# Kernel optimization log

Measured on AMD Instinct MI355X. Metric: run time of the kernel, lower is better.

## Reference

```python
import jax, jax.numpy as jnp
import numpy as np

D = 256  # rst_input_dim


def _gru_cell(x, h, W_ih, W_hh, b_ih, b_hh):
    # x, h: (..., D); W_*: (3D, D); PyTorch GRU gate order: r, z, n
    gi = x @ W_ih.T + b_ih          # (..., 3D)
    gh = h @ W_hh.T + b_hh
    i_r, i_z, i_n = jnp.split(gi, 3, axis=-1)
    h_r, h_z, h_n = jnp.split(gh, 3, axis=-1)
    r = jax.nn.sigmoid(i_r + h_r)
    z = jax.nn.sigmoid(i_z + h_z)
    n = jnp.tanh(i_n + r * h_n)
    return (1.0 - z) * n + z * h


def setup_inputs() -> dict:
    key = jax.random.key(0)
    ks = jax.random.split(key, 5)
    B, L = 32, 4096
    s = 1.0 / np.sqrt(D)
    return {
        "leaf_embeds": jax.random.normal(ks[0], (B, L, D), dtype=jnp.float32),
        "W_ih": jax.random.normal(ks[1], (3 * D, D), dtype=jnp.float32) * s,
        "W_hh": jax.random.normal(ks[2], (3 * D, D), dtype=jnp.float32) * s,
        "b_ih": jax.random.normal(ks[3], (3 * D,), dtype=jnp.float32) * s,
        "b_hh": jax.random.normal(ks[4], (3 * D,), dtype=jnp.float32) * s,
    }


def reference(leaf_embeds, W_ih, W_hh, b_ih, b_hh):
    # Post-order traversal of a perfect binary tree, batched level-by-level
    # (classic tree-RNN same-depth batching). Leaves: embed = EDU embedding,
    # hidden = zeros. Internal node: h0 = mean(h_left, h_right); run GRU over
    # the 2-step sequence [left_embed, right_embed]; out = mean of the two
    # GRU outputs; returned hidden = final GRU hidden.
    embeds = leaf_embeds                      # (B, N, D)
    hs = jnp.zeros_like(leaf_embeds)          # (B, N, D)
    n = embeds.shape[1]
    while n > 1:
        xL, xR = embeds[:, 0::2], embeds[:, 1::2]   # (B, n/2, D)
        hL, hR = hs[:, 0::2], hs[:, 1::2]
        h0 = 0.5 * (hL + hR)                         # mean of child hiddens
        h1 = _gru_cell(xL, h0, W_ih, W_hh, b_ih, b_hh)
        h2 = _gru_cell(xR, h1, W_ih, W_hh, b_ih, b_hh)
        embeds = 0.5 * (h1 + h2)                     # mean over seq outputs
        hs = h2
        n //= 2
    return embeds[:, 0]                              # (B, D): root embedding
```

## Files before the change

kernel.cpp:

```cpp
#include <hip/hip_runtime.h>
#include <hip/hip_bf16.h>
#include <stdint.h>

typedef _Float16 f16x8 __attribute__((ext_vector_type(8)));
typedef _Float16 f16x4 __attribute__((ext_vector_type(4)));
typedef float    f32x4 __attribute__((ext_vector_type(4)));

#define GLDS16(gptr, lptr) \
  __builtin_amdgcn_global_load_lds((const __attribute__((address_space(1))) void*)(gptr), \
                                   (__attribute__((address_space(3))) void*)(lptr), 16, 0, 0)

#define WAITV(N) asm volatile("s_waitcnt vmcnt(" #N ")" ::: "memory")

__device__ __forceinline__ int tile_off(int rb, int c, int sub) {
    return ((rb * 4 + c) * 8 + sub) * 512;
}

__global__ __launch_bounds__(256) void prepack_weights(
    const float* __restrict__ Wih, const float* __restrict__ Whh,
    const float* __restrict__ bih, const float* __restrict__ bhh,
    _Float16* __restrict__ WP, float* __restrict__ BC)
{
    if (blockIdx.x == 2048) {
        int i = threadIdx.x;
        BC[i]       = bih[i] + bhh[i];
        BC[256 + i] = bih[256 + i] + bhh[256 + i];
        BC[512 + i] = bih[512 + i];
        BC[768 + i] = bhh[512 + i];
        return;
    }
    int idx = blockIdx.x * 256 + threadIdx.x;
    int j   = idx & 7;
    int nl  = (idx >> 3) & 63;
    int sub = (idx >> 9) & 7;
    int g   = (idx >> 12) & 3;
    int d0b = (idx >> 14) & 3;
    int c   = idx >> 16;
    int k = c * 64 + sub * 8 + j;
    int d = d0b * 64 + nl;
    float v = 0.f;
    if (g == 0)      v = (k < 256) ? Wih[d * 256 + k]         : Whh[d * 256 + (k - 256)];
    else if (g == 1) v = (k < 256) ? Wih[(256 + d) * 256 + k] : Whh[(256 + d) * 256 + (k - 256)];
    else if (g == 2) v = (k < 256) ? Wih[(512 + d) * 256 + k] : 0.f;
    else             v = (k >= 256) ? Whh[(512 + d) * 256 + (k - 256)] : 0.f;
    WP[idx] = (_Float16)v;
}

__global__ __launch_bounds__(256) void convert_split(
    const float* __restrict__ leaf, _Float16* __restrict__ XE, _Float16* __restrict__ XO)
{
    int g = blockIdx.x * 256 + threadIdx.x;
    int u = g & 31;
    int row = g >> 5;
    const float* src = leaf + (size_t)row * 256 + u * 8;
    float4 a = *(const float4*)src;
    float4 b = *(const float4*)(src + 4);
    f16x8 p;
    p[0] = (_Float16)a.x; p[1] = (_Float16)a.y; p[2] = (_Float16)a.z; p[3] = (_Float16)a.w;
    p[4] = (_Float16)b.x; p[5] = (_Float16)b.y; p[6] = (_Float16)b.z; p[7] = (_Float16)b.w;
    int ro = row >> 1;
    _Float16* dst = (row & 1) ? XO : XE;
    *(f16x8*)(dst + tile_off(ro >> 6, u >> 3, u & 7) + (ro & 63) * 8) = p;
}

template<int MT, bool SWIZ>
__global__ __launch_bounds__(256, (MT == 8) ? 2 : 3) void gru_cell(
    const _Float16* __restrict__ Xsrc,
    const _Float16* __restrict__ Hsrc,
    const _Float16* __restrict__ WP,
    const float* __restrict__ BC,
    _Float16* __restrict__ Hout,
    _Float16* __restrict__ Ee, _Float16* __restrict__ Eo, _Float16* __restrict__ HP,
    int M)
{
    (void)M;
    constexpr int NBUF = (MT == 8) ? 2 : 3;
    constexpr int AROW = MT * 16 * 8;
    constexpr int ASZ  = 8 * AROW;
    __shared__ __align__(16) _Float16 Alds[NBUF * ASZ];

    const int tid  = threadIdx.x;
    int bm, d0b;
    if (SWIZ) {
        int xcd = blockIdx.x & 7, slot = blockIdx.x >> 3;
        d0b = slot & 3;
        bm  = (slot >> 2) * 8 + xcd;
    } else {
        bm = blockIdx.x >> 2; d0b = blockIdx.x & 3;
    }
    const int wave = tid >> 6, lane = tid & 63;
    const int quad = lane >> 4, lo = lane & 15;

    const bool has_h = (Hsrc != nullptr);
    const int nch = has_h ? 8 : 4;

    f32x4 acc[MT][4];
#pragma unroll
    for (int a = 0; a < MT; ++a)
#pragma unroll
        for (int b = 0; b < 4; ++b) acc[a][b] = (f32x4){0.f, 0.f, 0.f, 0.f};
    f16x4 hinvh[MT];

    auto loadB = [&](int c, f16x8 (&bb)[2][3]) {
        const size_t cb = (size_t)(c * 4 + d0b) * 4;
        const int col = (wave * 16 + lo) * 8;
#pragma unroll
        for (int ks = 0; ks < 2; ++ks) {
            const int subb = ks * 4 + quad;
#pragma unroll
            for (int slot = 0; slot < 3; ++slot) {
                int g = (slot == 2) ? ((c < 4) ? 2 : 3) : slot;
                bb[ks][slot] = *(const f16x8*)(WP + ((cb + g) * 8 + subb) * 512 + col);
            }
        }
    };

    auto issueA = [&](int c, int buf) {
        const _Float16* base = (c < 4) ? Xsrc : Hsrc;
        const int cc = c & 3;
        _Float16* Ab = Alds + buf * ASZ;
        constexpr int ND = MT / 2;
#pragma unroll
        for (int i = 0; i < ND; ++i) {
            int ai = wave * ND + i;
            int sub = (MT == 8) ? (ai >> 1) : ai;
            int mh  = (MT == 8) ? (ai & 1) : 0;
            GLDS16(base + tile_off(bm * (MT / 4) + mh, cc, sub) + lane * 8,
                   Ab + sub * AROW + mh * 512);
        }
    };

    auto compute = [&](int c, int buf, f16x8 (&bb)[2][3]) {
        const _Float16* Ab = Alds + buf * ASZ;
#pragma unroll
        for (int ks = 0; ks < 2; ++ks) {
            const int subb = ks * 4 + quad;
#pragma unroll
            for (int mt = 0; mt < MT; ++mt) {
                f16x8 a = *(const f16x8*)(Ab + subb * AROW + (mt * 16 + lo) * 8);
                acc[mt][0] = __builtin_amdgcn_mfma_f32_16x16x32_f16(a, bb[ks][0], acc[mt][0], 0, 0, 0);
                acc[mt][1] = __builtin_amdgcn_mfma_f32_16x16x32_f16(a, bb[ks][1], acc[mt][1], 0, 0, 0);
                if (c < 4)
                    acc[mt][2] = __builtin_amdgcn_mfma_f32_16x16x32_f16(a, bb[ks][2], acc[mt][2], 0, 0, 0);
                else
                    acc[mt][3] = __builtin_amdgcn_mfma_f32_16x16x32_f16(a, bb[ks][2], acc[mt][3], 0, 0, 0);
            }
        }
        if (has_h && c == 4 + d0b) {
            const int colw = wave * 16 + lo;
            const int sub = colw >> 3, j = colw & 7;
#pragma unroll
            for (int mt = 0; mt < MT; ++mt)
#pragma unroll
                for (int r = 0; r < 4; ++r)
                    hinvh[mt][r] = Ab[sub * AROW + (mt * 16 + quad * 4 + r) * 8 + j];
        }
    };

    if constexpr (MT == 8) {
        issueA(0, 0);
        for (int c = 0; c < nch; ++c) {
            __syncthreads();
            f16x8 bb[2][3];
            loadB(c, bb);
            __builtin_amdgcn_sched_barrier(0);
            if (c + 1 < nch) issueA(c + 1, (c + 1) & 1);
            compute(c, c & 1, bb);
        }
    } else {
        issueA(0, 0); issueA(1, 1);
        for (int c = 0; c < nch; ++c) {
            if (c < nch - 1) WAITV(2); else WAITV(0);
            __builtin_amdgcn_s_barrier();
            __builtin_amdgcn_sched_barrier(0);
            f16x8 bb[2][3];
            loadB(c, bb);
            __builtin_amdgcn_sched_barrier(0);
            if (c + 2 < nch) issueA(c + 2, (c + 2) % 3);
            compute(c, c % 3, bb);
        }
    }

    const int ld = wave * 16 + lo;
    const int d  = d0b * 64 + ld;
    const float brz0 = BC[d];
    const float brz1 = BC[256 + d];
    const float bni  = BC[512 + d];
    const float bnh  = BC[768 + d];
    constexpr int SROW = 72;
    constexpr int PR   = MT * 8;
    __syncthreads();
#pragma unroll
    for (int mt = 0; mt < MT; ++mt) {
        const int lr0 = mt * 16 + quad * 4;
        float hq[4];
#pragma unroll
        for (int r = 0; r < 4; ++r) {
            float hin = has_h ? (float)hinvh[mt][r] : 0.f;
            float rg = 1.f / (1.f + __expf(-(acc[mt][0][r] + brz0)));
            float zg = 1.f / (1.f + __expf(-(acc[mt][1][r] + brz1)));
            float ex = __expf(2.f * (acc[mt][2][r] + bni + rg * (acc[mt][3][r] + bnh)));
            float nv = 1.f - 2.f / (ex + 1.f);
            hq[r] = (1.f - zg) * nv + zg * hin;
            int lr = lr0 + r;
            if (Hout) {
                Alds[lr * SROW + ld] = (_Float16)hq[r];
            } else {
                Alds[(((lr & 1) * PR) + (lr >> 1)) * SROW + ld] =
                    (_Float16)(0.5f * (hin + hq[r]));
            }
        }
        if (!Hout) {
            Alds[(2 * PR + (lr0 >> 1)) * SROW + ld]     = (_Float16)(0.5f * (hq[0] + hq[1]));
            Alds[(2 * PR + (lr0 >> 1) + 1) * SROW + ld] = (_Float16)(0.5f * (hq[2] + hq[3]));
        }
    }
    __syncthreads();

    if (Hout) {
        constexpr int NU = MT * 128;
#pragma unroll
        for (int i = 0; i < NU / 256; ++i) {
            int uid = i * 256 + tid;
            int r = uid & 63, sub = (uid >> 6) & 7, mh = uid >> 9;
            f16x8 v = *(const f16x8*)&Alds[(mh * 64 + r) * SROW + sub * 8];
            *(f16x8*)(Hout + tile_off(bm * (MT / 4) + mh, d0b, sub) + r * 8) = v;
        }
    } else {
        constexpr int NU = 3 * PR * 8;
        const int rbE  = (MT == 8) ? bm : (bm >> 1);
        const int roff = (MT == 8) ? 0 : (bm & 1) * 32;
#pragma unroll
        for (int i = 0; i < NU / 256; ++i) {
            int uid = i * 256 + tid;
            int pr   = uid & (PR - 1);
            int rest = uid / PR;
            int sub = rest & 7, buf = rest >> 3;
            f16x8 v = *(const f16x8*)&Alds[(buf * PR + pr) * SROW + sub * 8];
            _Float16* dst = (buf == 0) ? Ee : (buf == 1) ? Eo : HP;
            *(f16x8*)(dst + tile_off(rbE, d0b, sub) + (roff + pr) * 8) = v;
        }
    }
}

__global__ __launch_bounds__(256) void final_out(
    const _Float16* __restrict__ XE, const _Float16* __restrict__ XO,
    float* __restrict__ out)
{
    int i = blockIdx.x * 256 + threadIdx.x;
    int j = i >> 8, col = i & 255;
    const _Float16* src = (j & 1) ? XO : XE;
    int r = j >> 1;
    out[i] = (float)src[tile_off(0, col >> 6, (col >> 3) & 7) + r * 8 + (col & 7)];
}

extern "C" void kernel_launch(void* const* d_in, const int* in_sizes, int n_in,
                              void* d_out, int out_size, void* d_ws, size_t ws_size,
                              hipStream_t stream) {
    const float* leaf = (const float*)d_in[0];
    const float* Wih  = (const float*)d_in[1];
    const float* Whh  = (const float*)d_in[2];
    const float* bih  = (const float*)d_in[3];
    const float* bhh  = (const float*)d_in[4];

    char* ws = (char*)d_ws;
    _Float16* WPp = (_Float16*)ws;
    _Float16* XAe = (_Float16*)(ws + (1ull  << 20));
    _Float16* XAo = (_Float16*)(ws + (33ull << 20));
    _Float16* XBe = (_Float16*)(ws + (65ull << 20));
    _Float16* XBo = (_Float16*)(ws + (81ull << 20));
    _Float16* H1  = (_Float16*)(ws + (97ull << 20));
    _Float16* HPb = (_Float16*)(ws + (129ull << 20));
    float*    BCp = (float*)(ws + (145ull << 20));

    prepack_weights<<<2049, 256, 0, stream>>>(Wih, Whh, bih, bhh, WPp, BCp);
    convert_split<<<16384, 256, 0, stream>>>(leaf, XAe, XAo);

    _Float16 *XeC = XAe, *XoC = XAo, *XeN = XBe, *XoN = XBo;
    const _Float16* hp = nullptr;
    int M = 65536;
    for (int lev = 0; lev < 12; ++lev) {
        if (M >= 8192) {
            int grid = (M / 128) * 4;
            gru_cell<8, true><<<grid, 256, 0, stream>>>(XeC, hp, WPp, BCp,
                                                        H1, nullptr, nullptr, nullptr, M);
            gru_cell<8, true><<<grid, 256, 0, stream>>>(XoC, H1, WPp, BCp,
                                                        nullptr, XeN, XoN, HPb, M);
        } else {
            int nbm = (M + 63) / 64;
            int grid = nbm * 4;
            if ((nbm & 7) == 0) {
                gru_cell<4, true><<<grid, 256, 0, stream>>>(XeC, hp, WPp, BCp,
                                                            H1, nullptr, nullptr, nullptr, M);
                gru_cell<4, true><<<grid, 256, 0, stream>>>(XoC, H1, WPp, BCp,
                                                            nullptr, XeN, XoN, HPb, M);
            } else {
                gru_cell<4, false><<<grid, 256, 0, stream>>>(XeC, hp, WPp, BCp,
                                                             H1, nullptr, nullptr, nullptr, M);
                gru_cell<4, false><<<grid, 256, 0, stream>>>(XoC, H1, WPp, BCp,
                                                             nullptr, XeN, XoN, HPb, M);
            }
        }
        hp = HPb;
        _Float16* t;
        t = XeC; XeC = XeN; XeN = t;
        t = XoC; XoC = XoN; XoN = t;
        M >>= 1;
    }
    final_out<<<32, 256, 0, stream>>>(XeC, XoC, (float*)d_out);
}
```

Baseline: 662.9 us.

## Fuse both GRU steps into one kernel for small tree levels

For levels 4 through 11, the two gru_cell launches per level are replaced by a single gru_tail16 kernel. Each block handles 16 rows across all 256 output columns, keeps h1 in LDS and registers, and runs the second GRU step without writing h1 to global memory. The last level writes the fp32 root output directly, so final_out is removed. This halves the launches and global round-trips on the latency-bound tail levels, at the cost of small grids (down to one block) that each read the full weight matrix per block.

```diff
diff --git a/kernel.cpp b/kernel.cpp
--- a/kernel.cpp
+++ b/kernel.cpp
@@ -64,7 +64,7 @@
 }
 
 template<int MT, bool SWIZ>
-__global__ __launch_bounds__(256, (MT == 8) ? 2 : 3) void gru_cell(
+__global__ __launch_bounds__(256, 2) void gru_cell(
     const _Float16* __restrict__ Xsrc,
     const _Float16* __restrict__ Hsrc,
     const _Float16* __restrict__ WP,
@@ -74,10 +74,9 @@
     int M)
 {
     (void)M;
-    constexpr int NBUF = (MT == 8) ? 2 : 3;
     constexpr int AROW = MT * 16 * 8;
     constexpr int ASZ  = 8 * AROW;
-    __shared__ __align__(16) _Float16 Alds[NBUF * ASZ];
+    __shared__ __align__(16) _Float16 Alds[2 * ASZ];
 
     const int tid  = threadIdx.x;
     int bm, d0b;
@@ -123,8 +122,7 @@
 #pragma unroll
         for (int i = 0; i < ND; ++i) {
             int ai = wave * ND + i;
-            int sub = (MT == 8) ? (ai >> 1) : ai;
-            int mh  = (MT == 8) ? (ai & 1) : 0;
+            int sub = ai >> 1, mh = ai & 1;
             GLDS16(base + tile_off(bm * (MT / 4) + mh, cc, sub) + lane * 8,
                    Ab + sub * AROW + mh * 512);
         }
@@ -157,28 +155,14 @@
         }
     };
 
-    if constexpr (MT == 8) {
-        issueA(0, 0);
-        for (int c = 0; c < nch; ++c) {
-            __syncthreads();
-            f16x8 bb[2][3];
-            loadB(c, bb);
-            __builtin_amdgcn_sched_barrier(0);
-            if (c + 1 < nch) issueA(c + 1, (c + 1) & 1);
-            compute(c, c & 1, bb);
-        }
-    } else {
-        issueA(0, 0); issueA(1, 1);
-        for (int c = 0; c < nch; ++c) {
-            if (c < nch - 1) WAITV(2); else WAITV(0);
-            __builtin_amdgcn_s_barrier();
-            __builtin_amdgcn_sched_barrier(0);
-            f16x8 bb[2][3];
-            loadB(c, bb);
-            __builtin_amdgcn_sched_barrier(0);
-            if (c + 2 < nch) issueA(c + 2, (c + 2) % 3);
-            compute(c, c % 3, bb);
-        }
+    issueA(0, 0);
+    for (int c = 0; c < nch; ++c) {
+        __syncthreads();
+        f16x8 bb[2][3];
+        loadB(c, bb);
+        __builtin_amdgcn_sched_barrier(0);
+        if (c + 1 < nch) issueA(c + 1, (c + 1) & 1);
+        compute(c, c & 1, bb);
     }
 
     const int ld = wave * 16 + lo;
@@ -228,8 +212,6 @@
         }
     } else {
         constexpr int NU = 3 * PR * 8;
-        const int rbE  = (MT == 8) ? bm : (bm >> 1);
-        const int roff = (MT == 8) ? 0 : (bm & 1) * 32;
 #pragma unroll
         for (int i = 0; i < NU / 256; ++i) {
             int uid = i * 256 + tid;
@@ -238,20 +220,178 @@
             int sub = rest & 7, buf = rest >> 3;
             f16x8 v = *(const f16x8*)&Alds[(buf * PR + pr) * SROW + sub * 8];
             _Float16* dst = (buf == 0) ? Ee : (buf == 1) ? Eo : HP;
-            *(f16x8*)(dst + tile_off(rbE, d0b, sub) + (roff + pr) * 8) = v;
-        }
-    }
-}
-
-__global__ __launch_bounds__(256) void final_out(
-    const _Float16* __restrict__ XE, const _Float16* __restrict__ XO,
-    float* __restrict__ out)
+            *(f16x8*)(dst + tile_off(bm, d0b, sub) + pr * 8) = v;
+        }
+    }
+}
+
+__global__ __launch_bounds__(256, 1) void gru_tail16(
+    const _Float16* __restrict__ Xe, const _Float16* __restrict__ Xo,
+    const _Float16* __restrict__ HPs,
+    const _Float16* __restrict__ WP, const float* __restrict__ BC,
+    _Float16* __restrict__ Ee, _Float16* __restrict__ Eo,
+    _Float16* __restrict__ HPd, float* __restrict__ out)
 {
-    int i = blockIdx.x * 256 + threadIdx.x;
-    int j = i >> 8, col = i & 255;
-    const _Float16* src = (j & 1) ? XO : XE;
-    int r = j >> 1;
-    out[i] = (float)src[tile_off(0, col >> 6, (col >> 3) & 7) + r * 8 + (col & 7)];
+    __shared__ __align__(16) _Float16 A[3][1024];
+    __shared__ __align__(16) _Float16 H1i[4][1024];
+
+    const int tid  = threadIdx.x;
+    const int wave = tid >> 6, lane = tid & 63;
+    const int quad = lane >> 4, lo = lane & 15;
+    const int bid  = blockIdx.x;
+    const int m0 = bid * 16, rb = m0 >> 6, ro = m0 & 63;
+
+    float brz0[4], brz1[4], bni[4], bnh[4];
+#pragma unroll
+    for (int nt = 0; nt < 4; ++nt) {
+        int d = wave * 64 + nt * 16 + lo;
+        brz0[nt] = BC[d];       brz1[nt] = BC[256 + d];
+        bni[nt]  = BC[512 + d]; bnh[nt]  = BC[768 + d];
+    }
+
+    f32x4 acc[4][4];
+    auto zacc = [&] {
+#pragma unroll
+        for (int nt = 0; nt < 4; ++nt)
+#pragma unroll
+            for (int g = 0; g < 4; ++g) acc[nt][g] = (f32x4){0.f, 0.f, 0.f, 0.f};
+    };
+
+    auto issueA = [&](const _Float16* base, int cc, int buf) {
+        const int i = wave >> 1;
+        GLDS16(base + tile_off(rb, cc, i * 4 + (lane >> 4)) + (ro + (lane & 15)) * 8,
+               &A[buf][i * 512]);
+    };
+
+    auto loadB = [&](int c, f16x8 (&bb)[2][4][3]) {
+#pragma unroll
+        for (int ks = 0; ks < 2; ++ks) {
+            const int subq = ks * 4 + quad;
+            const _Float16* wb = WP + (size_t)((c * 4 + wave) * 4) * 4096 + subq * 512;
+#pragma unroll
+            for (int nt = 0; nt < 4; ++nt) {
+                const int colb = (nt * 16 + lo) * 8;
+                bb[ks][nt][0] = *(const f16x8*)(wb + colb);
+                bb[ks][nt][1] = *(const f16x8*)(wb + 4096 + colb);
+                bb[ks][nt][2] = *(const f16x8*)(wb + ((c < 4) ? 2 : 3) * 4096 + colb);
+            }
+        }
+    };
+
+    auto mfmaC = [&](int c, const _Float16* Ab, f16x8 (&bb)[2][4][3]) {
+#pragma unroll
+        for (int ks = 0; ks < 2; ++ks) {
+            const int subq = ks * 4 + quad;
+            f16x8 a = *(const f16x8*)(Ab + subq * 128 + lo * 8);
+#pragma unroll
+            for (int nt = 0; nt < 4; ++nt) {
+                acc[nt][0] = __builtin_amdgcn_mfma_f32_16x16x32_f16(a, bb[ks][nt][0], acc[nt][0], 0, 0, 0);
+                acc[nt][1] = __builtin_amdgcn_mfma_f32_16x16x32_f16(a, bb[ks][nt][1], acc[nt][1], 0, 0, 0);
+                if (c < 4)
+                    acc[nt][2] = __builtin_amdgcn_mfma_f32_16x16x32_f16(a, bb[ks][nt][2], acc[nt][2], 0, 0, 0);
+                else
+                    acc[nt][3] = __builtin_amdgcn_mfma_f32_16x16x32_f16(a, bb[ks][nt][2], acc[nt][3], 0, 0, 0);
+            }
+        }
+    };
+
+    zacc();
+    float hin[4][4];
+    issueA(Xe, 0, 0);
+    issueA(Xe, 1, 1);
+    for (int c = 0; c < 8; ++c) {
+        if (c < 7) WAITV(1); else WAITV(0);
+        __builtin_amdgcn_s_barrier();
+        __builtin_amdgcn_sched_barrier(0);
+        f16x8 bb[2][4][3];
+        loadB(c, bb);
+        __builtin_amdgcn_sched_barrier(0);
+        if (c + 2 < 8) {
+            int cn = c + 2;
+            issueA((cn < 4) ? Xe : HPs, cn & 3, cn % 3);
+        }
+        const _Float16* Ab = A[c % 3];
+        mfmaC(c, Ab, bb);
+        if (c == 4 + wave) {
+#pragma unroll
+            for (int nt = 0; nt < 4; ++nt) {
+                const int sb = nt * 2 + (lo >> 3), j = lo & 7;
+#pragma unroll
+                for (int r = 0; r < 4; ++r)
+                    hin[nt][r] = (float)Ab[sb * 128 + (quad * 4 + r) * 8 + j];
+            }
+        }
+    }
+
+    __syncthreads();
+    float h1v[4][4];
+#pragma unroll
+    for (int nt = 0; nt < 4; ++nt) {
+        const int sb = nt * 2 + (lo >> 3), j = lo & 7;
+#pragma unroll
+        for (int r = 0; r < 4; ++r) {
+            float rg = 1.f / (1.f + __expf(-(acc[nt][0][r] + brz0[nt])));
+            float zg = 1.f / (1.f + __expf(-(acc[nt][1][r] + brz1[nt])));
+            float ex = __expf(2.f * (acc[nt][2][r] + bni[nt] + rg * (acc[nt][3][r] + bnh[nt])));
+            float nv = 1.f - 2.f / (ex + 1.f);
+            float h  = (1.f - zg) * nv + zg * hin[nt][r];
+            h1v[nt][r] = h;
+            H1i[wave][sb * 128 + (quad * 4 + r) * 8 + j] = (_Float16)h;
+        }
+    }
+    __syncthreads();
+
+    zacc();
+    issueA(Xo, 0, 0);
+    issueA(Xo, 1, 1);
+    for (int c = 0; c < 4; ++c) {
+        if (c < 3) WAITV(1); else WAITV(0);
+        __builtin_amdgcn_s_barrier();
+        __builtin_amdgcn_sched_barrier(0);
+        f16x8 bb[2][4][3];
+        loadB(c, bb);
+        __builtin_amdgcn_sched_barrier(0);
+        if (c + 2 < 4) issueA(Xo, c + 2, (c + 2) % 3);
+        mfmaC(c, A[c % 3], bb);
+    }
+#pragma unroll
+    for (int c = 4; c < 8; ++c) {
+        f16x8 bb[2][4][3];
+        loadB(c, bb);
+        mfmaC(c, &H1i[c - 4][0], bb);
+    }
+
+#pragma unroll
+    for (int nt = 0; nt < 4; ++nt) {
+        const int sb = nt * 2 + (lo >> 3), j = lo & 7;
+        float h2[4];
+#pragma unroll
+        for (int r = 0; r < 4; ++r) {
+            float rg = 1.f / (1.f + __expf(-(acc[nt][0][r] + brz0[nt])));
+            float zg = 1.f / (1.f + __expf(-(acc[nt][1][r] + brz1[nt])));
+            float ex = __expf(2.f * (acc[nt][2][r] + bni[nt] + rg * (acc[nt][3][r] + bnh[nt])));
+            float nv = 1.f - 2.f / (ex + 1.f);
+            h2[r] = (1.f - zg) * nv + zg * h1v[nt][r];
+        }
+        if (out) {
+#pragma unroll
+            for (int r = 0; r < 4; ++r)
+                out[(size_t)(m0 + quad * 4 + r) * 256 + wave * 64 + nt * 16 + lo] =
+                    0.5f * (h1v[nt][r] + h2[r]);
+        } else {
+            const int rbE   = bid >> 3;
+            const int rbase = (bid & 7) * 8 + quad * 2;
+            const int toff  = tile_off(rbE, wave, sb);
+#pragma unroll
+            for (int r = 0; r < 4; ++r) {
+                _Float16* dst = (r & 1) ? Eo : Ee;
+                dst[toff + (rbase + (r >> 1)) * 8 + j] =
+                    (_Float16)(0.5f * (h1v[nt][r] + h2[r]));
+            }
+            HPd[toff + rbase * 8 + j]       = (_Float16)(0.5f * (h2[0] + h2[1]));
+            HPd[toff + (rbase + 1) * 8 + j] = (_Float16)(0.5f * (h2[2] + h2[3]));
+        }
+    }
 }
 
 extern "C" void kernel_launch(void* const* d_in, const int* in_sizes, int n_in,
@@ -270,6 +410,7 @@
     _Float16* XBe = (_Float16*)(ws + (65ull << 20));
     _Float16* XBo = (_Float16*)(ws + (81ull << 20));
     _Float16* H1  = (_Float16*)(ws + (97ull << 20));
+    _Float16* HP2 = (_Float16*)(ws + (113ull << 20));
     _Float16* HPb = (_Float16*)(ws + (129ull << 20));
     float*    BCp = (float*)(ws + (145ull << 20));
 
@@ -279,33 +420,29 @@
     _Float16 *XeC = XAe, *XoC = XAo, *XeN = XBe, *XoN = XBo;
     const _Float16* hp = nullptr;
     int M = 65536;
-    for (int lev = 0; lev < 12; ++lev) {
-        if (M >= 8192) {
-            int grid = (M / 128) * 4;
-            gru_cell<8, true><<<grid, 256, 0, stream>>>(XeC, hp, WPp, BCp,
-                                                        H1, nullptr, nullptr, nullptr, M);
-            gru_cell<8, true><<<grid, 256, 0, stream>>>(XoC, H1, WPp, BCp,
-                                                        nullptr, XeN, XoN, HPb, M);
-        } else {
-            int nbm = (M + 63) / 64;
-            int grid = nbm * 4;
-            if ((nbm & 7) == 0) {
-                gru_cell<4, true><<<grid, 256, 0, stream>>>(XeC, hp, WPp, BCp,
-                                                            H1, nullptr, nullptr, nullptr, M);
-                gru_cell<4, true><<<grid, 256, 0, stream>>>(XoC, H1, WPp, BCp,
-                                                            nullptr, XeN, XoN, HPb, M);
-            } else {
-                gru_cell<4, false><<<grid, 256, 0, stream>>>(XeC, hp, WPp, BCp,
-                                                             H1, nullptr, nullptr, nullptr, M);
-                gru_cell<4, false><<<grid, 256, 0, stream>>>(XoC, H1, WPp, BCp,
-                                                             nullptr, XeN, XoN, HPb, M);
-            }
-        }
+    for (int lev = 0; lev < 4; ++lev) {
+        int grid = (M / 128) * 4;
+        gru_cell<8, true><<<grid, 256, 0, stream>>>(XeC, hp, WPp, BCp,
+                                                    H1, nullptr, nullptr, nullptr, M);
+        gru_cell<8, true><<<grid, 256, 0, stream>>>(XoC, H1, WPp, BCp,
+                                                    nullptr, XeN, XoN, HPb, M);
         hp = HPb;
         _Float16* t;
         t = XeC; XeC = XeN; XeN = t;
         t = XoC; XoC = XoN; XoN = t;
         M >>= 1;
     }
-    final_out<<<32, 256, 0, stream>>>(XeC, XoC, (float*)d_out);
-}
+
+    for (int lev = 4; lev <= 11; ++lev) {
+        int nb = (65536 >> lev) / 16;
+        _Float16* Xe = (lev & 1) ? XBe : XAe;
+        _Float16* Xo = (lev & 1) ? XBo : XAo;
+        _Float16* De = (lev & 1) ? XAe : XBe;
+        _Float16* Do = (lev & 1) ? XAo : XBo;
+        _Float16* HPsrc = (lev & 1) ? HP2 : HPb;
+        _Float16* HPdst = (lev & 1) ? HPb : HP2;
+        float* op = (lev == 11) ? (float*)d_out : nullptr;
+        gru_tail16<<<nb, 256, 0, stream>>>(Xe, Xo, HPsrc, WPp, BCp,
+                                           De, Do, HPdst, op);
+    }
+}
```

Result: slower. 751.1 us (+13.3%).

## Fuse small tree levels into one persistent kernel with grid barriers

Applied to the files above, without the earlier changes.

Levels 4 through 11, where the row count is small, now run inside a single persistent kernel of 256 blocks. Blocks synchronize between GRU half-steps with an atomic-counter grid barrier, and the final output copy is folded into the same kernel. This removes roughly 17 small kernel launches and their launch gaps, which dominate when work per level is tiny. The cost is spin-wait barrier overhead and a reliance on all 256 blocks being co-resident. HP buffers now ping-pong to avoid read/write hazards within the fused kernel.

```diff
diff --git a/kernel.cpp b/kernel.cpp
--- a/kernel.cpp
+++ b/kernel.cpp
@@ -19,7 +19,7 @@
 __global__ __launch_bounds__(256) void prepack_weights(
     const float* __restrict__ Wih, const float* __restrict__ Whh,
     const float* __restrict__ bih, const float* __restrict__ bhh,
-    _Float16* __restrict__ WP, float* __restrict__ BC)
+    _Float16* __restrict__ WP, float* __restrict__ BC, int* __restrict__ CNT)
 {
     if (blockIdx.x == 2048) {
         int i = threadIdx.x;
@@ -27,6 +27,7 @@
         BC[256 + i] = bih[256 + i] + bhh[256 + i];
         BC[512 + i] = bih[512 + i];
         BC[768 + i] = bhh[512 + i];
+        if (i == 0) *CNT = 0;
         return;
     }
     int idx = blockIdx.x * 256 + threadIdx.x;
@@ -64,7 +65,7 @@
 }
 
 template<int MT, bool SWIZ>
-__global__ __launch_bounds__(256, (MT == 8) ? 2 : 3) void gru_cell(
+__global__ __launch_bounds__(256, 2) void gru_cell(
     const _Float16* __restrict__ Xsrc,
     const _Float16* __restrict__ Hsrc,
     const _Float16* __restrict__ WP,
@@ -74,10 +75,9 @@
     int M)
 {
     (void)M;
-    constexpr int NBUF = (MT == 8) ? 2 : 3;
     constexpr int AROW = MT * 16 * 8;
     constexpr int ASZ  = 8 * AROW;
-    __shared__ __align__(16) _Float16 Alds[NBUF * ASZ];
+    __shared__ __align__(16) _Float16 Alds[2 * ASZ];
 
     const int tid  = threadIdx.x;
     int bm, d0b;
@@ -123,8 +123,7 @@
 #pragma unroll
         for (int i = 0; i < ND; ++i) {
             int ai = wave * ND + i;
-            int sub = (MT == 8) ? (ai >> 1) : ai;
-            int mh  = (MT == 8) ? (ai & 1) : 0;
+            int sub = ai >> 1, mh = ai & 1;
             GLDS16(base + tile_off(bm * (MT / 4) + mh, cc, sub) + lane * 8,
                    Ab + sub * AROW + mh * 512);
         }
@@ -157,28 +156,14 @@
         }
     };
 
-    if constexpr (MT == 8) {
-        issueA(0, 0);
-        for (int c = 0; c < nch; ++c) {
-            __syncthreads();
-            f16x8 bb[2][3];
-            loadB(c, bb);
-            __builtin_amdgcn_sched_barrier(0);
-            if (c + 1 < nch) issueA(c + 1, (c + 1) & 1);
-            compute(c, c & 1, bb);
-        }
-    } else {
-        issueA(0, 0); issueA(1, 1);
-        for (int c = 0; c < nch; ++c) {
-            if (c < nch - 1) WAITV(2); else WAITV(0);
-            __builtin_amdgcn_s_barrier();
-            __builtin_amdgcn_sched_barrier(0);
-            f16x8 bb[2][3];
-            loadB(c, bb);
-            __builtin_amdgcn_sched_barrier(0);
-            if (c + 2 < nch) issueA(c + 2, (c + 2) % 3);
-            compute(c, c % 3, bb);
-        }
+    issueA(0, 0);
+    for (int c = 0; c < nch; ++c) {
+        __syncthreads();
+        f16x8 bb[2][3];
+        loadB(c, bb);
+        __builtin_amdgcn_sched_barrier(0);
+        if (c + 1 < nch) issueA(c + 1, (c + 1) & 1);
+        compute(c, c & 1, bb);
     }
 
     const int ld = wave * 16 + lo;
@@ -228,8 +213,152 @@
         }
     } else {
         constexpr int NU = 3 * PR * 8;
-        const int rbE  = (MT == 8) ? bm : (bm >> 1);
-        const int roff = (MT == 8) ? 0 : (bm & 1) * 32;
+#pragma unroll
+        for (int i = 0; i < NU / 256; ++i) {
+            int uid = i * 256 + tid;
+            int pr   = uid & (PR - 1);
+            int rest = uid / PR;
+            int sub = rest & 7, buf = rest >> 3;
+            f16x8 v = *(const f16x8*)&Alds[(buf * PR + pr) * SROW + sub * 8];
+            _Float16* dst = (buf == 0) ? Ee : (buf == 1) ? Eo : HP;
+            *(f16x8*)(dst + tile_off(bm, d0b, sub) + pr * 8) = v;
+        }
+    }
+}
+
+__device__ void cell4(const _Float16* __restrict__ Xsrc,
+                      const _Float16* __restrict__ Hsrc,
+                      const _Float16* __restrict__ WP,
+                      const float* __restrict__ BC,
+                      _Float16* Hout, _Float16* Ee, _Float16* Eo, _Float16* HP,
+                      int bm, int d0b, int tid, _Float16* Alds)
+{
+    constexpr int MT   = 4;
+    constexpr int AROW = 512;
+    constexpr int ASZ  = 4096;
+    const int wave = tid >> 6, lane = tid & 63;
+    const int quad = lane >> 4, lo = lane & 15;
+
+    f32x4 acc[MT][4];
+#pragma unroll
+    for (int a = 0; a < MT; ++a)
+#pragma unroll
+        for (int b = 0; b < 4; ++b) acc[a][b] = (f32x4){0.f, 0.f, 0.f, 0.f};
+    f16x4 hinvh[MT];
+
+    auto loadB = [&](int c, f16x8 (&bb)[2][3]) {
+        const size_t cb = (size_t)(c * 4 + d0b) * 4;
+        const int col = (wave * 16 + lo) * 8;
+#pragma unroll
+        for (int ks = 0; ks < 2; ++ks) {
+            const int subb = ks * 4 + quad;
+#pragma unroll
+            for (int slot = 0; slot < 3; ++slot) {
+                int g = (slot == 2) ? ((c < 4) ? 2 : 3) : slot;
+                bb[ks][slot] = *(const f16x8*)(WP + ((cb + g) * 8 + subb) * 512 + col);
+            }
+        }
+    };
+
+    auto issueA = [&](int c, int buf) {
+        const _Float16* base = (c < 4) ? Xsrc : Hsrc;
+        const int cc = c & 3;
+        _Float16* Ab = Alds + buf * ASZ;
+#pragma unroll
+        for (int i = 0; i < 2; ++i) {
+            int sub = wave * 2 + i;
+            GLDS16(base + tile_off(bm, cc, sub) + lane * 8, Ab + sub * AROW);
+        }
+    };
+
+    auto compute = [&](int c, int buf, f16x8 (&bb)[2][3]) {
+        const _Float16* Ab = Alds + buf * ASZ;
+#pragma unroll
+        for (int ks = 0; ks < 2; ++ks) {
+            const int subb = ks * 4 + quad;
+#pragma unroll
+            for (int mt = 0; mt < MT; ++mt) {
+                f16x8 a = *(const f16x8*)(Ab + subb * AROW + (mt * 16 + lo) * 8);
+                acc[mt][0] = __builtin_amdgcn_mfma_f32_16x16x32_f16(a, bb[ks][0], acc[mt][0], 0, 0, 0);
+                acc[mt][1] = __builtin_amdgcn_mfma_f32_16x16x32_f16(a, bb[ks][1], acc[mt][1], 0, 0, 0);
+                if (c < 4)
+                    acc[mt][2] = __builtin_amdgcn_mfma_f32_16x16x32_f16(a, bb[ks][2], acc[mt][2], 0, 0, 0);
+                else
+                    acc[mt][3] = __builtin_amdgcn_mfma_f32_16x16x32_f16(a, bb[ks][2], acc[mt][3], 0, 0, 0);
+            }
+        }
+        if (c == 4 + d0b) {
+            const int colw = wave * 16 + lo;
+            const int sub = colw >> 3, j = colw & 7;
+#pragma unroll
+            for (int mt = 0; mt < MT; ++mt)
+#pragma unroll
+                for (int r = 0; r < 4; ++r)
+                    hinvh[mt][r] = Ab[sub * AROW + (mt * 16 + quad * 4 + r) * 8 + j];
+        }
+    };
+
+    issueA(0, 0); issueA(1, 1);
+    for (int c = 0; c < 8; ++c) {
+        if (c < 7) WAITV(2); else WAITV(0);
+        __builtin_amdgcn_s_barrier();
+        __builtin_amdgcn_sched_barrier(0);
+        f16x8 bb[2][3];
+        loadB(c, bb);
+        __builtin_amdgcn_sched_barrier(0);
+        if (c + 2 < 8) issueA(c + 2, (c + 2) % 3);
+        compute(c, c % 3, bb);
+    }
+
+    const int ld = wave * 16 + lo;
+    const int d  = d0b * 64 + ld;
+    const float brz0 = BC[d];
+    const float brz1 = BC[256 + d];
+    const float bni  = BC[512 + d];
+    const float bnh  = BC[768 + d];
+    constexpr int SROW = 72;
+    constexpr int PR   = 32;
+    __syncthreads();
+#pragma unroll
+    for (int mt = 0; mt < MT; ++mt) {
+        const int lr0 = mt * 16 + quad * 4;
+        float hq[4];
+#pragma unroll
+        for (int r = 0; r < 4; ++r) {
+            float hin = (float)hinvh[mt][r];
+            float rg = 1.f / (1.f + __expf(-(acc[mt][0][r] + brz0)));
+            float zg = 1.f / (1.f + __expf(-(acc[mt][1][r] + brz1)));
+            float ex = __expf(2.f * (acc[mt][2][r] + bni + rg * (acc[mt][3][r] + bnh)));
+            float nv = 1.f - 2.f / (ex + 1.f);
+            hq[r] = (1.f - zg) * nv + zg * hin;
+            int lr = lr0 + r;
+            if (Hout) {
+                Alds[lr * SROW + ld] = (_Float16)hq[r];
+            } else {
+                Alds[(((lr & 1) * PR) + (lr >> 1)) * SROW + ld] =
+                    (_Float16)(0.5f * (hin + hq[r]));
+            }
+        }
+        if (!Hout) {
+            Alds[(2 * PR + (lr0 >> 1)) * SROW + ld]     = (_Float16)(0.5f * (hq[0] + hq[1]));
+            Alds[(2 * PR + (lr0 >> 1) + 1) * SROW + ld] = (_Float16)(0.5f * (hq[2] + hq[3]));
+        }
+    }
+    __syncthreads();
+
+    if (Hout) {
+        constexpr int NU = 512;
+#pragma unroll
+        for (int i = 0; i < NU / 256; ++i) {
+            int uid = i * 256 + tid;
+            int r = uid & 63, sub = (uid >> 6) & 7;
+            f16x8 v = *(const f16x8*)&Alds[r * SROW + sub * 8];
+            *(f16x8*)(Hout + tile_off(bm, d0b, sub) + r * 8) = v;
+        }
+    } else {
+        constexpr int NU = 3 * PR * 8;
+        const int rbE  = bm >> 1;
+        const int roff = (bm & 1) * 32;
 #pragma unroll
         for (int i = 0; i < NU / 256; ++i) {
             int uid = i * 256 + tid;
@@ -243,15 +372,52 @@
     }
 }
 
-__global__ __launch_bounds__(256) void final_out(
-    const _Float16* __restrict__ XE, const _Float16* __restrict__ XO,
-    float* __restrict__ out)
+__device__ __forceinline__ void gbar(int* cnt, int target, int tid) {
+    __syncthreads();
+    if (tid == 0) {
+        __threadfence();
+        atomicAdd(cnt, 1);
+        while (__hip_atomic_load(cnt, __ATOMIC_RELAXED, __HIP_MEMORY_SCOPE_AGENT) < target)
+            __builtin_amdgcn_s_sleep(2);
+        __threadfence();
+    }
+    __syncthreads();
+}
+
+__global__ __launch_bounds__(256, 1) void gru_tail_persist(
+    _Float16* XAe, _Float16* XAo, _Float16* XBe, _Float16* XBo,
+    const _Float16* __restrict__ WP, const float* __restrict__ BC,
+    _Float16* H1, _Float16* HPa, _Float16* HPb2, int* cnt, float* out)
 {
-    int i = blockIdx.x * 256 + threadIdx.x;
-    int j = i >> 8, col = i & 255;
-    const _Float16* src = (j & 1) ? XO : XE;
-    int r = j >> 1;
-    out[i] = (float)src[tile_off(0, col >> 6, (col >> 3) & 7) + r * 8 + (col & 7)];
+    __shared__ __align__(16) _Float16 Alds[3 * 4096];
+    const int tid = threadIdx.x;
+    const int vb  = blockIdx.x;
+    const int bm = vb >> 2, d0b = vb & 3;
+    int bt = 0;
+
+    for (int lev = 4; lev <= 11; ++lev) {
+        const int M   = 65536 >> lev;
+        const int nv  = ((M + 63) >> 6) * 4;
+        _Float16* Xe = (lev & 1) ? XBe : XAe;
+        _Float16* Xo = (lev & 1) ? XBo : XAo;
+        _Float16* De = (lev & 1) ? XAe : XBe;
+        _Float16* Do = (lev & 1) ? XAo : XBo;
+        _Float16* HPsrc = (lev & 1) ? HPb2 : HPa;
+        _Float16* HPdst = (lev & 1) ? HPa : HPb2;
+        if (vb < nv)
+            cell4(Xe, HPsrc, WP, BC, H1, nullptr, nullptr, nullptr, bm, d0b, tid, Alds);
+        bt += 256; gbar(cnt, bt, tid);
+        if (vb < nv)
+            cell4(Xo, H1, WP, BC, nullptr, De, Do, HPdst, bm, d0b, tid, Alds);
+        bt += 256; gbar(cnt, bt, tid);
+    }
+    if (vb < 32) {
+        int col = tid;
+        const _Float16* src = (vb & 1) ? XAo : XAe;
+        int r = vb >> 1;
+        out[vb * 256 + col] =
+            (float)src[tile_off(0, col >> 6, (col >> 3) & 7) + r * 8 + (col & 7)];
+    }
 }
 
 extern "C" void kernel_launch(void* const* d_in, const int* in_sizes, int n_in,
@@ -270,42 +436,30 @@
     _Float16* XBe = (_Float16*)(ws + (65ull << 20));
     _Float16* XBo = (_Float16*)(ws + (81ull << 20));
     _Float16* H1  = (_Float16*)(ws + (97ull << 20));
+    _Float16* HP2 = (_Float16*)(ws + (113ull << 20));
     _Float16* HPb = (_Float16*)(ws + (129ull << 20));
     float*    BCp = (float*)(ws + (145ull << 20));
-
-    prepack_weights<<<2049, 256, 0, stream>>>(Wih, Whh, bih, bhh, WPp, BCp);
+    int*      CNT = (int*)(ws + (145ull << 20) + 8192);
+
+    prepack_weights<<<2049, 256, 0, stream>>>(Wih, Whh, bih, bhh, WPp, BCp, CNT);
     convert_split<<<16384, 256, 0, stream>>>(leaf, XAe, XAo);
 
     _Float16 *XeC = XAe, *XoC = XAo, *XeN = XBe, *XoN = XBo;
     const _Float16* hp = nullptr;
     int M = 65536;
-    for (int lev = 0; lev < 12; ++lev) {
-        if (M >= 8192) {
-            int grid = (M / 128) * 4;
-            gru_cell<8, true><<<grid, 256, 0, stream>>>(XeC, hp, WPp, BCp,
-                                                        H1, nullptr, nullptr, nullptr, M);
-            gru_cell<8, true><<<grid, 256, 0, stream>>>(XoC, H1, WPp, BCp,
-                                                        nullptr, XeN, XoN, HPb, M);
-        } else {
-            int nbm = (M + 63) / 64;
-            int grid = nbm * 4;
-            if ((nbm & 7) == 0) {
-                gru_cell<4, true><<<grid, 256, 0, stream>>>(XeC, hp, WPp, BCp,
-                                                            H1, nullptr, nullptr, nullptr, M);
-                gru_cell<4, true><<<grid, 256, 0, stream>>>(XoC, H1, WPp, BCp,
-                                                            nullptr, XeN, XoN, HPb, M);
-            } else {
-                gru_cell<4, false><<<grid, 256, 0, stream>>>(XeC, hp, WPp, BCp,
-                                                             H1, nullptr, nullptr, nullptr, M);
-                gru_cell<4, false><<<grid, 256, 0, stream>>>(XoC, H1, WPp, BCp,
-                                                             nullptr, XeN, XoN, HPb, M);
-            }
-        }
+    for (int lev = 0; lev < 4; ++lev) {
+        int grid = (M / 128) * 4;
+        gru_cell<8, true><<<grid, 256, 0, stream>>>(XeC, hp, WPp, BCp,
+                                                    H1, nullptr, nullptr, nullptr, M);
+        gru_cell<8, true><<<grid, 256, 0, stream>>>(XoC, H1, WPp, BCp,
+                                                    nullptr, XeN, XoN, HPb, M);
         hp = HPb;
         _Float16* t;
         t = XeC; XeC = XeN; XeN = t;
         t = XoC; XoC = XoN; XoN = t;
         M >>= 1;
     }
-    final_out<<<32, 256, 0, stream>>>(XeC, XoC, (float*)d_out);
-}
+
+    gru_tail_persist<<<256, 256, 0, stream>>>(XAe, XAo, XBe, XBo, WPp, BCp,
+                                              H1, HPb, HP2, CNT, (float*)d_out);
+}
```

After: 874.5 us. +31.9%, slower.
